# Kernel optimization log

Hardware: AMD Instinct MI355X
Metric: run time of the kernel (lower is better)

The kernel has to match this reference:

```python
import jax, jax.numpy as jnp
import numpy as np

LOSS_IDX = jnp.array([0, 1])    # loss_indices from __init__
BASIS_IDX = jnp.array([0, 1])   # dtw_mapping_basis (x, y)


def _dtw_path(cost):
    """Classic DTW DP + backtrack on cost [N, M].
    Returns padded alignment path (a, b) of length N+M-1 with validity mask.
    DP is run as an anti-diagonal wavefront scan (L = N+M-1 steps)."""
    N, M = cost.shape
    L = N + M - 1
    inf = jnp.float32(jnp.inf)
    i_idx = jnp.arange(N)

    def diag_step(carry, k):
        prev1, prev2 = carry  # diagonals k-1 and k-2, indexed by row i
        j = k - i_idx
        valid = (j >= 0) & (j < M)
        c = cost[i_idx, jnp.clip(j, 0, M - 1)]
        up = jnp.concatenate([jnp.full((1,), inf), prev1[:-1]])  # D[i-1, j]
        dg = jnp.concatenate([jnp.full((1,), inf), prev2[:-1]])  # D[i-1, j-1]
        lf = prev1                                               # D[i, j-1]
        best = jnp.minimum(jnp.minimum(up, dg), lf)
        best = jnp.where(jnp.isinf(best), jnp.float32(0.0), best)  # (0,0) seed
        cur = jnp.where(valid, c + best, inf)
        return (cur, prev1), cur

    init = (jnp.full((N,), inf), jnp.full((N,), inf))
    _, diags = jax.lax.scan(diag_step, init, jnp.arange(L))  # [L, N]: D[i,j] = diags[i+j, i]

    def getD(i, j):
        ok = (i >= 0) & (j >= 0)
        return jnp.where(ok, diags[jnp.clip(i + j, 0, L - 1), jnp.clip(i, 0, N - 1)], inf)

    def bt_step(carry, _):
        i, j, done = carry
        emit_valid = jnp.logical_not(done)
        cand = jnp.stack([getD(i - 1, j - 1), getD(i - 1, j), getD(i, j - 1)])
        m = jnp.argmin(cand)  # 0: diag, 1: up, 2: left
        ni = jnp.where(m == 2, i, i - 1)
        nj = jnp.where(m == 1, j, j - 1)
        done2 = done | ((i == 0) & (j == 0))
        ni = jnp.where(done2, 0, ni)
        nj = jnp.where(done2, 0, nj)
        return (ni, nj, done2), (i, j, emit_valid)

    init_bt = (jnp.int32(N - 1), jnp.int32(M - 1), jnp.bool_(False))
    _, (a, b, valid) = jax.lax.scan(bt_step, init_bt, None, length=L)
    return a, b, valid


def _dtw_loss_single(pred, targ, subcoef):
    # DTW alignment is computed on detached (numpy in torch) basis coords.
    p = jax.lax.stop_gradient(pred)[:, BASIS_IDX]
    t = jax.lax.stop_gradient(targ)[:, BASIS_IDX]
    # euclidean pairwise distance cost [N, M]
    cost = jnp.sqrt(jnp.sum((p[:, None, :] - t[None, :, :]) ** 2, axis=-1))
    a, b, valid = _dtw_path(cost)
    d = jnp.abs(pred[a][:, LOSS_IDX] - targ[b][:, LOSS_IDX]) * subcoef  # [L, 2]
    return jnp.sum(d * valid[:, None].astype(d.dtype))


def setup_inputs() -> dict:
    key = jax.random.key(0)
    k1, k2 = jax.random.split(key)
    B, N, M, F = 32, 1024, 1024, 4
    preds = jax.random.normal(k1, (B, N, F), dtype=jnp.float32)
    targs = jax.random.normal(k2, (B, M, F), dtype=jnp.float32)
    subcoef = jnp.ones((2,), dtype=jnp.float32)
    return {"preds": preds, "targs": targs, "subcoef": subcoef}


def reference(preds, targs, subcoef):
    per_sample = jax.vmap(_dtw_loss_single, in_axes=(0, 0, None))(preds, targs, subcoef)
    return jnp.sum(per_sample)
```

## Files before the change

kernel.cpp:

```cpp
#include <hip/hip_runtime.h>
#include <math.h>

#define BATCH 32
#define NN 1024
#define MM 1024
#define RR 4
#define CC 4
#define LANES 64
#define NWAVE 4
#define TPB (MM / 4)
#define NSUP (TPB + LANES - 1)
#define LAG 72
#define TOT (NSUP + (NWAVE - 1) * LAG)
#define DEPTH 32
#define DEC_WORDS_PER_BATCH ((NN / 4) * (MM / 4))
#define DEC_BYTES ((size_t)BATCH * DEC_WORDS_PER_BATCH * 4)
#define REQ_WS DEC_BYTES
#define LPATH (NN + MM - 1)

__global__ void init_kernel(float* out) { out[0] = 0.0f; }

__device__ inline void bt_walk4(const unsigned* __restrict__ sdec, int roff,
                                int iLow, int& i, int& j, int& n,
                                unsigned* __restrict__ path)
{
    int ri = i >> 2, jc = j >> 2;
    unsigned w = sdec[(ri - roff) * 256 + jc];
    while (true) {
        const int base = (ri - roff) * 256 + jc;
        const unsigned wl = sdec[(jc > 0)    ? base - 1   : base];
        const unsigned wu = sdec[(ri > roff) ? base - 256 : base];
        const unsigned wd = sdec[(ri > roff && jc > 0) ? base - 257 : base];
        bool done = false, susp = false;
        while (true) {
            path[n++] = ((unsigned)i << 16) | (unsigned)j;
            if ((i | j) == 0) { done = true; break; }
            const unsigned m = (w >> (((i & 3) * 4 + (j & 3)) * 2)) & 3u;
            i -= (m != 2u); j -= (m != 1u);
            if (i < iLow) { susp = true; break; }
            if ((i >> 2) != ri || (j >> 2) != jc) break;
        }
        if (done || susp) break;
        const int nri = i >> 2, njc = j >> 2;
        w = (nri == ri) ? wl : ((njc == jc) ? wu : wd);
        ri = nri; jc = njc;
    }
}

__global__ __launch_bounds__(256, 1) void dtw_fused(
    const float* __restrict__ preds, const float* __restrict__ targs,
    const float* __restrict__ subcoef, unsigned* __restrict__ dec,
    float* __restrict__ out)
{
    const int b = blockIdx.x, t = threadIdx.x;
    const int l = t & 63, w = t >> 6;
    const float INF = __builtin_inff();

    __shared__ float pxA[NN], pyA[NN], txA[MM], tyA[MM];
    __shared__ float4 ring[NWAVE - 1][DEPTH];
    __shared__ unsigned sdec[128 * 256];
    __shared__ unsigned path[LPATH + 1];
    __shared__ int sI, sJ, sN;
    __shared__ float wsum[NWAVE];

    for (int it = 0; it < NN / 256; ++it) {
        const int idx = it * 256 + t;
        const float4 p4 = ((const float4*)preds)[(size_t)b * NN + idx];
        pxA[idx] = p4.x; pyA[idx] = p4.y;
        const float4 t4 = ((const float4*)targs)[(size_t)b * MM + idx];
        txA[idx] = t4.x; tyA[idx] = t4.y;
    }
    __syncthreads();

    const int i0 = (w << 8) + (l << 2);
    const float4 px4 = ((const float4*)pxA)[i0 >> 2];
    const float4 py4 = ((const float4*)pyA)[i0 >> 2];
    const float px[RR] = {px4.x, px4.y, px4.z, px4.w};
    const float py[RR] = {py4.x, py4.y, py4.z, py4.w};
    unsigned* __restrict__ decT =
        dec + (size_t)b * DEC_WORDS_PER_BATCH + (size_t)(i0 >> 2) * TPB;

    float Dp[RR], Dbot[CC], bv[CC];
    #pragma unroll
    for (int r = 0; r < RR; ++r) Dp[r] = INF;
    #pragma unroll
    for (int c = 0; c < CC; ++c) { Dbot[c] = INF; bv[c] = INF; }
    float bndRet = (w == 0 && l == 0) ? 0.0f : INF;
    float4 gcur = make_float4(INF, INF, INF, INF);
    float4 tx4 = ((const float4*)txA)[0], ty4 = ((const float4*)tyA)[0];

    for (int u = 0; u < TOT; ++u) {
        const int ul = u - LAG * w;
        if (l == 0) {
            const bool gb = (w > 0) && (ul >= 0) && (ul < TPB);
            bv[0] = gb ? gcur.x : INF; bv[1] = gb ? gcur.y : INF;
            bv[2] = gb ? gcur.z : INF; bv[3] = gb ? gcur.w : INF;
        }
        const bool act = (ul >= l) && (ul < l + TPB);
        if (act) {
            const int j0 = CC * (ul - l);
            const float cx[CC] = {tx4.x, tx4.y, tx4.z, tx4.w};
            const float cy[CC] = {ty4.x, ty4.y, ty4.z, ty4.w};
            float cost[RR][CC];
            #pragma unroll
            for (int c = 0; c < CC; ++c)
                #pragma unroll
                for (int r = 0; r < RR; ++r) {
                    const float dx = px[r] - cx[c], dy = py[r] - cy[c];
                    cost[r][c] = __builtin_amdgcn_sqrtf(dx * dx + dy * dy);
                }
            unsigned word = 0;
            #pragma unroll
            for (int c = 0; c < CC; ++c) {
                float up = bv[c];
                float dg = (c == 0) ? bndRet : bv[c - 1];
                #pragma unroll
                for (int r = 0; r < RR; ++r) {
                    const float lf = Dp[r];
                    const unsigned m = (dg <= up && dg <= lf) ? 0u
                                     : ((up <= lf) ? 1u : 2u);
                    const float D = cost[r][c] + fminf(dg, fminf(up, lf));
                    word |= m << ((r * 4 + c) * 2);
                    dg = lf; up = D; Dp[r] = D;
                }
                Dbot[c] = up;
            }
            decT[j0 >> 2] = word;
            if (l == LANES - 1 && w < NWAVE - 1)
                ring[w][ul & (DEPTH - 1)] =
                    make_float4(Dbot[0], Dbot[1], Dbot[2], Dbot[3]);
        }
        bndRet = bv[CC - 1];
        #pragma unroll
        for (int c = 0; c < CC; ++c) bv[c] = __shfl_up(Dbot[c], 1);
        const int un = ul + 1;
        if (un >= l && un < l + TPB) {
            const int jn = CC * (un - l);
            tx4 = ((const float4*)txA)[jn >> 2];
            ty4 = ((const float4*)tyA)[jn >> 2];
        }
        if (l == 0 && w > 0 && un >= 0 && un < TPB)
            gcur = ring[w - 1][(un + 63) & (DEPTH - 1)];
        if ((u & 7) == 7) __syncthreads();
    }

    __threadfence_block();
    __syncthreads();

    const unsigned* __restrict__ decB = dec + (size_t)b * DEC_WORDS_PER_BATCH;
    {
        uint4* s4 = (uint4*)sdec;
        const uint4* g4 = (const uint4*)(decB + 128 * 256);
        for (int k = t; k < 8192; k += 256) s4[k] = g4[k];
    }
    __syncthreads();
    if (t == 0) {
        int i = NN - 1, j = MM - 1, n = 0;
        bt_walk4(sdec, 128, 512, i, j, n, path);
        sI = i; sJ = j; sN = n;
    }
    __syncthreads();
    {
        uint4* s4 = (uint4*)sdec;
        const uint4* g4 = (const uint4*)decB;
        for (int k = t; k < 8192; k += 256) s4[k] = g4[k];
    }
    __syncthreads();
    if (t == 0) {
        int i = sI, j = sJ, n = sN;
        bt_walk4(sdec, 0, 0, i, j, n, path);
        sN = n;
    }
    __syncthreads();

    const float sc0 = subcoef[0], sc1 = subcoef[1];
    const int n = sN;
    float acc = 0.0f;
    for (int p = t; p < n; p += 256) {
        const unsigned e = path[p];
        const int i = (int)(e >> 16), j = (int)(e & 0xffffu);
        acc += fabsf(pxA[i] - txA[j]) * sc0 + fabsf(pyA[i] - tyA[j]) * sc1;
    }
    #pragma unroll
    for (int o = 32; o > 0; o >>= 1) acc += __shfl_down(acc, o);
    if ((t & 63) == 0) wsum[t >> 6] = acc;
    __syncthreads();
    if (t == 0) atomicAdd(out, (wsum[0] + wsum[1]) + (wsum[2] + wsum[3]));
}

__global__ __launch_bounds__(256) void dtw_fallback(
    const float* __restrict__ preds, const float* __restrict__ targs,
    const float* __restrict__ subcoef, unsigned* __restrict__ dec,
    float* __restrict__ out)
{
    const int b = blockIdx.x;
    const int t = threadIdx.x;
    const float INF = __builtin_inff();
    __shared__ float px[NN], py[NN];
    __shared__ float txy[2 * MM];
    __shared__ float bbuf[2][256];

    for (int it = 0; it < NN / 256; ++it) {
        const int idx = it * 256 + t;
        const float4 p4 = ((const float4*)preds)[(size_t)b * NN + idx];
        px[idx] = p4.x; py[idx] = p4.y;
        const float4 t4 = ((const float4*)targs)[(size_t)b * MM + idx];
        txy[2 * idx] = t4.x; txy[2 * idx + 1] = t4.y;
    }
    bbuf[0][t] = INF; bbuf[1][t] = INF;
    __syncthreads();

    float pxr[4], pyr[4], Dp[4];
    #pragma unroll
    for (int r = 0; r < 4; ++r) {
        pxr[r] = px[4 * t + r]; pyr[r] = py[4 * t + r]; Dp[r] = INF;
    }
    float dgB = (t == 0) ? 0.0f : INF;
    unsigned packed = 0;
    unsigned* decB = dec + (size_t)b * 65536;
    for (int s = 0; s < MM + 255; ++s) {
        const int j = s - t;
        const float upB = (t == 0) ? INF : bbuf[(s + 1) & 1][t - 1];
        if (j >= 0 && j < MM) {
            const float txj = txy[2 * j], tyj = txy[2 * j + 1];
            float up = upB, dg = dgB;
            unsigned mbits = 0;
            #pragma unroll
            for (int r = 0; r < 4; ++r) {
                const float dx = pxr[r] - txj, dy = pyr[r] - tyj;
                const float c = sqrtf(dx * dx + dy * dy);
                const float lf = Dp[r];
                const unsigned m = (dg <= up && dg <= lf) ? 0u
                                 : ((up <= lf) ? 1u : 2u);
                mbits |= m << (r * 8 + (j & 3) * 2);
                const float Dc = c + fminf(up, fminf(dg, lf));
                dg = lf; up = Dc; Dp[r] = Dc;
            }
            packed |= mbits;
            if ((j & 3) == 3) { decB[(unsigned)t * 256 + (j >> 2)] = packed; packed = 0; }
            bbuf[s & 1][t] = Dp[3];
        }
        dgB = upB;
        __syncthreads();
    }
    __threadfence_block();
    __syncthreads();
    if (t == 0) {
        const float sc0 = subcoef[0], sc1 = subcoef[1];
        int i = NN - 1, jj = MM - 1;
        float loss = 0.0f;
        int ti = i >> 2, tj = jj >> 2;
        unsigned wv = decB[ti * 256 + tj];
        while (true) {
            const int tjl = (tj > 0) ? tj - 1 : 0;
            const int til = (ti > 0) ? ti - 1 : 0;
            const unsigned wl = decB[ti * 256 + tjl];
            const unsigned wu = decB[til * 256 + tj];
            const unsigned wd = decB[til * 256 + tjl];
            bool done = false;
            while (true) {
                loss += fabsf(px[i] - txy[2 * jj]) * sc0
                      + fabsf(py[i] - txy[2 * jj + 1]) * sc1;
                if ((i | jj) == 0) { done = true; break; }
                const unsigned m = (wv >> (((i & 3) * 4 + (jj & 3)) * 2)) & 3u;
                i -= (m != 2u); jj -= (m != 1u);
                if ((i >> 2) != ti || (jj >> 2) != tj) break;
            }
            if (done) break;
            const int nti = i >> 2, ntj = jj >> 2;
            wv = (nti == ti) ? wl : ((ntj == tj) ? wu : wd);
            ti = nti; tj = ntj;
        }
        atomicAdd(out, loss);
    }
}

extern "C" void kernel_launch(void* const* d_in, const int* in_sizes, int n_in,
                              void* d_out, int out_size, void* d_ws, size_t ws_size,
                              hipStream_t stream) {
    const float* preds   = (const float*)d_in[0];
    const float* targs   = (const float*)d_in[1];
    const float* subcoef = (const float*)d_in[2];
    float* out = (float*)d_out;
    unsigned* dec = (unsigned*)d_ws;

    init_kernel<<<1, 1, 0, stream>>>(out);
    if (ws_size >= REQ_WS) {
        dtw_fused<<<BATCH, 256, 0, stream>>>(preds, targs, subcoef, dec, out);
    } else {
        dtw_fallback<<<BATCH, 256, 0, stream>>>(preds, targs, subcoef, dec, out);
    }
}
```

Measured before the change: 598.2 us.

## Store decision words diagonal-packed per wave and backtrack in four bands

Each wave now keeps its decision words for eight wavefront steps in registers and writes them in a skewed, diagonal-packed layout once per 8-step group. The goal is coalesced global stores, since consecutive lanes on one diagonal land in adjacent words. Backtracking now runs over four per-wave bands of 16K words instead of two 32K-word halves, so shared memory use shrinks at the cost of more index arithmetic in the lookups. The lane shift moves to a DPP row-shift intrinsic, and the argmin test is rewritten to compare against the computed minimum.

```diff
diff --git a/kernel.cpp b/kernel.cpp
--- a/kernel.cpp
+++ b/kernel.cpp
@@ -11,40 +11,35 @@
 #define TPB (MM / 4)
 #define NSUP (TPB + LANES - 1)
 #define LAG 72
-#define TOT (NSUP + (NWAVE - 1) * LAG)
+#define TOT8 67
 #define DEPTH 32
-#define DEC_WORDS_PER_BATCH ((NN / 4) * (MM / 4))
+#define WORDS_PER_WAVE 16384
+#define DEC_WORDS_PER_BATCH (NWAVE * WORDS_PER_WAVE)
 #define DEC_BYTES ((size_t)BATCH * DEC_WORDS_PER_BATCH * 4)
 #define REQ_WS DEC_BYTES
 #define LPATH (NN + MM - 1)
 
 __global__ void init_kernel(float* out) { out[0] = 0.0f; }
 
-__device__ inline void bt_walk4(const unsigned* __restrict__ sdec, int roff,
-                                int iLow, int& i, int& j, int& n,
-                                unsigned* __restrict__ path)
-{
-    int ri = i >> 2, jc = j >> 2;
-    unsigned w = sdec[(ri - roff) * 256 + jc];
-    while (true) {
-        const int base = (ri - roff) * 256 + jc;
-        const unsigned wl = sdec[(jc > 0)    ? base - 1   : base];
-        const unsigned wu = sdec[(ri > roff) ? base - 256 : base];
-        const unsigned wd = sdec[(ri > roff && jc > 0) ? base - 257 : base];
-        bool done = false, susp = false;
-        while (true) {
-            path[n++] = ((unsigned)i << 16) | (unsigned)j;
-            if ((i | j) == 0) { done = true; break; }
-            const unsigned m = (w >> (((i & 3) * 4 + (j & 3)) * 2)) & 3u;
-            i -= (m != 2u); j -= (m != 1u);
-            if (i < iLow) { susp = true; break; }
-            if ((i >> 2) != ri || (j >> 2) != jc) break;
-        }
-        if (done || susp) break;
-        const int nri = i >> 2, njc = j >> 2;
-        w = (nri == ri) ? wl : ((njc == jc) ? wu : wd);
-        ri = nri; jc = njc;
-    }
+__device__ __forceinline__ float wave_shr1(float v, float fb) {
+    return __int_as_float(__builtin_amdgcn_update_dpp(
+        __float_as_int(fb), __float_as_int(v), 0x138, 0xf, 0xf, false));
+}
+
+__device__ __forceinline__ int pkoff(int d) {
+    if (d <= 63) return (d * (d + 1)) >> 1;
+    if (d <= 256) return 2016 + ((d - 63) << 6);
+    const int e = d - 256;
+    return 14368 + 63 * e - ((e * (e - 1)) >> 1);
+}
+__device__ __forceinline__ unsigned ldw(const unsigned* __restrict__ sdec,
+                                        int lr, int jc) {
+    int d = jc + lr;
+    d = d < 0 ? 0 : (d > 318 ? 318 : d);
+    const int lo = d > 255 ? d - 255 : 0;
+    const int hi = d < 63 ? d : 63;
+    const int l = lr < lo ? lo : (lr > hi ? hi : lr);
+    return sdec[pkoff(d) + l - lo];
 }
 
 __global__ __launch_bounds__(256, 1) void dtw_fused(
@@ -58,7 +53,7 @@
 
     __shared__ float pxA[NN], pyA[NN], txA[MM], tyA[MM];
     __shared__ float4 ring[NWAVE - 1][DEPTH];
-    __shared__ unsigned sdec[128 * 256];
+    __shared__ unsigned sdec[WORDS_PER_WAVE];
     __shared__ unsigned path[LPATH + 1];
     __shared__ int sI, sJ, sN;
     __shared__ float wsum[NWAVE];
@@ -77,8 +72,8 @@
     const float4 py4 = ((const float4*)pyA)[i0 >> 2];
     const float px[RR] = {px4.x, px4.y, px4.z, px4.w};
     const float py[RR] = {py4.x, py4.y, py4.z, py4.w};
-    unsigned* __restrict__ decT =
-        dec + (size_t)b * DEC_WORDS_PER_BATCH + (size_t)(i0 >> 2) * TPB;
+    unsigned* __restrict__ decW =
+        dec + (size_t)b * DEC_WORDS_PER_BATCH + (size_t)w * WORDS_PER_WAVE;
 
     float Dp[RR], Dbot[CC], bv[CC];
     #pragma unroll
@@ -88,90 +83,117 @@
     float bndRet = (w == 0 && l == 0) ? 0.0f : INF;
     float4 gcur = make_float4(INF, INF, INF, INF);
     float4 tx4 = ((const float4*)txA)[0], ty4 = ((const float4*)tyA)[0];
-
-    for (int u = 0; u < TOT; ++u) {
-        const int ul = u - LAG * w;
-        if (l == 0) {
-            const bool gb = (w > 0) && (ul >= 0) && (ul < TPB);
-            bv[0] = gb ? gcur.x : INF; bv[1] = gb ? gcur.y : INF;
-            bv[2] = gb ? gcur.z : INF; bv[3] = gb ? gcur.w : INF;
-        }
-        const bool act = (ul >= l) && (ul < l + TPB);
-        if (act) {
-            const int j0 = CC * (ul - l);
-            const float cx[CC] = {tx4.x, tx4.y, tx4.z, tx4.w};
-            const float cy[CC] = {ty4.x, ty4.y, ty4.z, ty4.w};
-            float cost[RR][CC];
+    unsigned wreg[8];
+
+    for (int u8 = 0; u8 < TOT8; ++u8) {
+        #pragma unroll
+        for (int dd = 0; dd < 8; ++dd) {
+            const int u = u8 * 8 + dd;
+            const int ul = u - LAG * w;
+            if (l == 0) {
+                const bool gb = (w > 0) && (ul >= 0) && (ul < TPB);
+                bv[0] = gb ? gcur.x : INF; bv[1] = gb ? gcur.y : INF;
+                bv[2] = gb ? gcur.z : INF; bv[3] = gb ? gcur.w : INF;
+            }
+            const bool act = (ul >= l) && (ul < l + TPB);
+            if (act) {
+                const float cx[CC] = {tx4.x, tx4.y, tx4.z, tx4.w};
+                const float cy[CC] = {ty4.x, ty4.y, ty4.z, ty4.w};
+                float cost[RR][CC];
+                #pragma unroll
+                for (int c = 0; c < CC; ++c)
+                    #pragma unroll
+                    for (int r = 0; r < RR; ++r) {
+                        const float dx = px[r] - cx[c], dy = py[r] - cy[c];
+                        cost[r][c] = __builtin_amdgcn_sqrtf(dx * dx + dy * dy);
+                    }
+                unsigned word = 0;
+                #pragma unroll
+                for (int c = 0; c < CC; ++c) {
+                    float up = bv[c];
+                    float dg = (c == 0) ? bndRet : bv[c - 1];
+                    #pragma unroll
+                    for (int r = 0; r < RR; ++r) {
+                        const float lf = Dp[r];
+                        const float best = fminf(dg, fminf(up, lf));
+                        const unsigned m = (best == dg) ? 0u
+                                         : ((best == up) ? 1u : 2u);
+                        const float D = cost[r][c] + best;
+                        word |= m << ((r * 4 + c) * 2);
+                        dg = lf; up = D; Dp[r] = D;
+                    }
+                    Dbot[c] = up;
+                }
+                wreg[dd] = word;
+                if (l == LANES - 1 && w < NWAVE - 1)
+                    ring[w][ul & (DEPTH - 1)] =
+                        make_float4(Dbot[0], Dbot[1], Dbot[2], Dbot[3]);
+            }
+            bndRet = bv[CC - 1];
             #pragma unroll
-            for (int c = 0; c < CC; ++c)
-                #pragma unroll
-                for (int r = 0; r < RR; ++r) {
-                    const float dx = px[r] - cx[c], dy = py[r] - cy[c];
-                    cost[r][c] = __builtin_amdgcn_sqrtf(dx * dx + dy * dy);
+            for (int c = 0; c < CC; ++c) bv[c] = wave_shr1(Dbot[c], INF);
+            const int un = ul + 1;
+            if (un >= l && un < l + TPB) {
+                const int jn = CC * (un - l);
+                tx4 = ((const float4*)txA)[jn >> 2];
+                ty4 = ((const float4*)tyA)[jn >> 2];
+            }
+            if (l == 0 && w > 0 && un >= 0 && un < TPB)
+                gcur = ring[w - 1][(un + 63) & (DEPTH - 1)];
+        }
+        const int ulbase = u8 * 8 - LAG * w;
+        #pragma unroll
+        for (int dd = 0; dd < 8; ++dd) {
+            const int d = ulbase + dd;
+            if (d >= 0 && d <= 318 && (unsigned)(d - l) < 256u) {
+                const int lo = d > 255 ? d - 255 : 0;
+                decW[pkoff(d) + l - lo] = wreg[dd];
+            }
+        }
+        __syncthreads();
+    }
+
+    __threadfence_block();
+    __syncthreads();
+
+    const unsigned* __restrict__ decB = dec + (size_t)b * DEC_WORDS_PER_BATCH;
+    if (t == 0) { sI = NN - 1; sJ = MM - 1; sN = 0; }
+    __syncthreads();
+    for (int band = NWAVE - 1; band >= 0; --band) {
+        {
+            uint4* s4 = (uint4*)sdec;
+            const uint4* g4 = (const uint4*)(decB + band * WORDS_PER_WAVE);
+            for (int k = t; k < WORDS_PER_WAVE / 4; k += 256) s4[k] = g4[k];
+        }
+        __syncthreads();
+        if (t == 0 && sI >= (band << 8)) {
+            int i = sI, j = sJ, n = sN;
+            const int iLow = band << 8, roff = band << 6;
+            int lr = (i >> 2) - roff, jc = j >> 2;
+            unsigned wcur = ldw(sdec, lr, jc);
+            while (true) {
+                const unsigned wl = ldw(sdec, lr, jc - 1);
+                const unsigned wu = ldw(sdec, lr - 1, jc);
+                const unsigned wd = ldw(sdec, lr - 1, jc - 1);
+                bool done = false, susp = false;
+                while (true) {
+                    path[n++] = ((unsigned)i << 16) | (unsigned)j;
+                    if ((i | j) == 0) { done = true; break; }
+                    const unsigned m =
+                        (wcur >> (((i & 3) * 4 + (j & 3)) * 2)) & 3u;
+                    i -= (m != 2u); j -= (m != 1u);
+                    if (i < iLow) { susp = true; break; }
+                    if (((i >> 2) - roff) != lr || (j >> 2) != jc) break;
                 }
-            unsigned word = 0;
-            #pragma unroll
-            for (int c = 0; c < CC; ++c) {
-                float up = bv[c];
-                float dg = (c == 0) ? bndRet : bv[c - 1];
-                #pragma unroll
-                for (int r = 0; r < RR; ++r) {
-                    const float lf = Dp[r];
-                    const unsigned m = (dg <= up && dg <= lf) ? 0u
-                                     : ((up <= lf) ? 1u : 2u);
-                    const float D = cost[r][c] + fminf(dg, fminf(up, lf));
-                    word |= m << ((r * 4 + c) * 2);
-                    dg = lf; up = D; Dp[r] = D;
-                }
-                Dbot[c] = up;
-            }
-            decT[j0 >> 2] = word;
-            if (l == LANES - 1 && w < NWAVE - 1)
-                ring[w][ul & (DEPTH - 1)] =
-                    make_float4(Dbot[0], Dbot[1], Dbot[2], Dbot[3]);
-        }
-        bndRet = bv[CC - 1];
-        #pragma unroll
-        for (int c = 0; c < CC; ++c) bv[c] = __shfl_up(Dbot[c], 1);
-        const int un = ul + 1;
-        if (un >= l && un < l + TPB) {
-            const int jn = CC * (un - l);
-            tx4 = ((const float4*)txA)[jn >> 2];
-            ty4 = ((const float4*)tyA)[jn >> 2];
-        }
-        if (l == 0 && w > 0 && un >= 0 && un < TPB)
-            gcur = ring[w - 1][(un + 63) & (DEPTH - 1)];
-        if ((u & 7) == 7) __syncthreads();
-    }
-
-    __threadfence_block();
-    __syncthreads();
-
-    const unsigned* __restrict__ decB = dec + (size_t)b * DEC_WORDS_PER_BATCH;
-    {
-        uint4* s4 = (uint4*)sdec;
-        const uint4* g4 = (const uint4*)(decB + 128 * 256);
-        for (int k = t; k < 8192; k += 256) s4[k] = g4[k];
-    }
-    __syncthreads();
-    if (t == 0) {
-        int i = NN - 1, j = MM - 1, n = 0;
-        bt_walk4(sdec, 128, 512, i, j, n, path);
-        sI = i; sJ = j; sN = n;
-    }
-    __syncthreads();
-    {
-        uint4* s4 = (uint4*)sdec;
-        const uint4* g4 = (const uint4*)decB;
-        for (int k = t; k < 8192; k += 256) s4[k] = g4[k];
-    }
-    __syncthreads();
-    if (t == 0) {
-        int i = sI, j = sJ, n = sN;
-        bt_walk4(sdec, 0, 0, i, j, n, path);
-        sN = n;
-    }
-    __syncthreads();
+                if (done || susp) break;
+                const int nlr = (i >> 2) - roff, njc = j >> 2;
+                wcur = (nlr == lr) ? wl : ((njc == jc) ? wu : wd);
+                lr = nlr; jc = njc;
+            }
+            sI = i; sJ = j; sN = n;
+        }
+        __syncthreads();
+    }
 
     const float sc0 = subcoef[0], sc1 = subcoef[1];
     const int n = sN;
```

Result: slower. 702.8 us (+17.5%).

## Replace periodic block barriers with per-wave progress flags in DTW wavefront

Applied to the files above, without the earlier changes.

Removes the __syncthreads issued every 8 steps in the wavefront DP loop. Each producer wave now publishes a release-stored progress counter, and each consumer wave spin-waits with acquire loads only when it needs boundary values that have not yet arrived. This lets waves drift independently instead of meeting at a barrier. It also simplifies the argmin selection by comparing against the computed minimum, and makes the target-coordinate loads unconditional with a clamped index. The spin loop with s_sleep adds polling latency and depends on a correct ordering between the ring writes and the flag store.

```diff
diff --git a/kernel.cpp b/kernel.cpp
--- a/kernel.cpp
+++ b/kernel.cpp
@@ -11,7 +11,7 @@
 #define TPB (MM / 4)
 #define NSUP (TPB + LANES - 1)
 #define LAG 72
-#define TOT (NSUP + (NWAVE - 1) * LAG)
+#define TOT (TPB + LANES - 1 + (NWAVE - 1) * LAG)
 #define DEPTH 32
 #define DEC_WORDS_PER_BATCH ((NN / 4) * (MM / 4))
 #define DEC_BYTES ((size_t)BATCH * DEC_WORDS_PER_BATCH * 4)
@@ -57,7 +57,8 @@
     const float INF = __builtin_inff();
 
     __shared__ float pxA[NN], pyA[NN], txA[MM], tyA[MM];
-    __shared__ float4 ring[NWAVE - 1][DEPTH];
+    __shared__ float ring[NWAVE - 1][DEPTH * 4];
+    __shared__ int prog[NWAVE - 1];
     __shared__ unsigned sdec[128 * 256];
     __shared__ unsigned path[LPATH + 1];
     __shared__ int sI, sJ, sN;
@@ -70,6 +71,7 @@
         const float4 t4 = ((const float4*)targs)[(size_t)b * MM + idx];
         txA[idx] = t4.x; tyA[idx] = t4.y;
     }
+    if (t < NWAVE - 1) prog[t] = 0;
     __syncthreads();
 
     const int i0 = (w << 8) + (l << 2);
@@ -86,19 +88,15 @@
     #pragma unroll
     for (int c = 0; c < CC; ++c) { Dbot[c] = INF; bv[c] = INF; }
     float bndRet = (w == 0 && l == 0) ? 0.0f : INF;
-    float4 gcur = make_float4(INF, INF, INF, INF);
     float4 tx4 = ((const float4*)txA)[0], ty4 = ((const float4*)tyA)[0];
+    float rv0 = INF, rv1 = INF, rv2 = INF, rv3 = INF;
+    int cachedProg = 0;
 
     for (int u = 0; u < TOT; ++u) {
         const int ul = u - LAG * w;
-        if (l == 0) {
-            const bool gb = (w > 0) && (ul >= 0) && (ul < TPB);
-            bv[0] = gb ? gcur.x : INF; bv[1] = gb ? gcur.y : INF;
-            bv[2] = gb ? gcur.z : INF; bv[3] = gb ? gcur.w : INF;
-        }
+        const int un = ul + 1;
         const bool act = (ul >= l) && (ul < l + TPB);
         if (act) {
-            const int j0 = CC * (ul - l);
             const float cx[CC] = {tx4.x, tx4.y, tx4.z, tx4.w};
             const float cy[CC] = {ty4.x, ty4.y, ty4.z, ty4.w};
             float cost[RR][CC];
@@ -117,31 +115,51 @@
                 #pragma unroll
                 for (int r = 0; r < RR; ++r) {
                     const float lf = Dp[r];
-                    const unsigned m = (dg <= up && dg <= lf) ? 0u
-                                     : ((up <= lf) ? 1u : 2u);
-                    const float D = cost[r][c] + fminf(dg, fminf(up, lf));
+                    const float best = fminf(dg, fminf(up, lf));
+                    const unsigned m = (best == dg) ? 0u
+                                     : ((best == up) ? 1u : 2u);
+                    const float D = cost[r][c] + best;
                     word |= m << ((r * 4 + c) * 2);
                     dg = lf; up = D; Dp[r] = D;
                 }
                 Dbot[c] = up;
             }
-            decT[j0 >> 2] = word;
-            if (l == LANES - 1 && w < NWAVE - 1)
-                ring[w][ul & (DEPTH - 1)] =
-                    make_float4(Dbot[0], Dbot[1], Dbot[2], Dbot[3]);
+            decT[ul - l] = word;
+            if (l == LANES - 1 && w < NWAVE - 1) {
+                volatile float* rp = &ring[w][(ul & (DEPTH - 1)) * 4];
+                rp[0] = Dbot[0]; rp[1] = Dbot[1];
+                rp[2] = Dbot[2]; rp[3] = Dbot[3];
+                if ((ul & 7) == 7 || ul == NSUP - 1)
+                    __hip_atomic_store(&prog[w], ul + 1, __ATOMIC_RELEASE,
+                                       __HIP_MEMORY_SCOPE_WORKGROUP);
+            }
         }
         bndRet = bv[CC - 1];
         #pragma unroll
         for (int c = 0; c < CC; ++c) bv[c] = __shfl_up(Dbot[c], 1);
-        const int un = ul + 1;
-        if (un >= l && un < l + TPB) {
-            const int jn = CC * (un - l);
-            tx4 = ((const float4*)txA)[jn >> 2];
-            ty4 = ((const float4*)tyA)[jn >> 2];
-        }
-        if (l == 0 && w > 0 && un >= 0 && un < TPB)
-            gcur = ring[w - 1][(un + 63) & (DEPTH - 1)];
-        if ((u & 7) == 7) __syncthreads();
+        if (w > 0) {
+            const int need = un + 64;
+            if (need >= 64 && need <= NSUP && cachedProg < need) {
+                do {
+                    __builtin_amdgcn_s_sleep(1);
+                    cachedProg = __hip_atomic_load(&prog[w - 1],
+                        __ATOMIC_ACQUIRE, __HIP_MEMORY_SCOPE_WORKGROUP);
+                } while (cachedProg < need);
+            }
+            const volatile float* rp =
+                &ring[w - 1][(((un + 63) & (DEPTH - 1))) * 4];
+            rv0 = rp[0]; rv1 = rp[1]; rv2 = rp[2]; rv3 = rp[3];
+        }
+        const bool useRing = (w > 0) && (un >= 0) && (un < TPB);
+        const float m0 = useRing ? rv0 : INF;
+        const float m1 = useRing ? rv1 : INF;
+        const float m2 = useRing ? rv2 : INF;
+        const float m3 = useRing ? rv3 : INF;
+        if (l == 0) { bv[0] = m0; bv[1] = m1; bv[2] = m2; bv[3] = m3; }
+        int jn = CC * (un - l);
+        jn = jn < 0 ? 0 : (jn > MM - 4 ? MM - 4 : jn);
+        tx4 = ((const float4*)txA)[jn >> 2];
+        ty4 = ((const float4*)tyA)[jn >> 2];
     }
 
     __threadfence_block();
```

After: 713.2 us. 19.2% more time.

## Pack two batch items per 512-thread block with chunked backtrack staging

Applied to the files above, without the earlier changes.

Each block now handles two batch samples using two independent 256-thread halves, so the grid drops from 32 blocks to 16. To fit two samples in LDS, the backtrack decision table is staged in 60-row chunks instead of two 128-row halves, and pred coordinates are read straight from global memory rather than staged in shared memory. Argmin selection is also recomputed from the min value. The per-sample serial wavefront stays the same, so two samples now share one CU and its issue slots and synchronisation, and the backtrack needs more staging passes.

```diff
diff --git a/kernel.cpp b/kernel.cpp
--- a/kernel.cpp
+++ b/kernel.cpp
@@ -11,12 +11,13 @@
 #define TPB (MM / 4)
 #define NSUP (TPB + LANES - 1)
 #define LAG 72
-#define TOT (NSUP + (NWAVE - 1) * LAG)
+#define TOT (TPB + LANES - 1 + (NWAVE - 1) * LAG)
 #define DEPTH 32
 #define DEC_WORDS_PER_BATCH ((NN / 4) * (MM / 4))
 #define DEC_BYTES ((size_t)BATCH * DEC_WORDS_PER_BATCH * 4)
 #define REQ_WS DEC_BYTES
 #define LPATH (NN + MM - 1)
+#define PH 60
 
 __global__ void init_kernel(float* out) { out[0] = 0.0f; }
 
@@ -47,38 +48,43 @@
     }
 }
 
-__global__ __launch_bounds__(256, 1) void dtw_fused(
+__global__ __launch_bounds__(512, 1) void dtw_fused2(
     const float* __restrict__ preds, const float* __restrict__ targs,
     const float* __restrict__ subcoef, unsigned* __restrict__ dec,
     float* __restrict__ out)
 {
-    const int b = blockIdx.x, t = threadIdx.x;
-    const int l = t & 63, w = t >> 6;
+    const int t = threadIdx.x;
+    const int sb = t >> 8;
+    const int tt = t & 255;
+    const int l = tt & 63, w = tt >> 6;
+    const int b = 2 * blockIdx.x + sb;
     const float INF = __builtin_inff();
 
-    __shared__ float pxA[NN], pyA[NN], txA[MM], tyA[MM];
-    __shared__ float4 ring[NWAVE - 1][DEPTH];
-    __shared__ unsigned sdec[128 * 256];
-    __shared__ unsigned path[LPATH + 1];
-    __shared__ int sI, sJ, sN;
-    __shared__ float wsum[NWAVE];
-
-    for (int it = 0; it < NN / 256; ++it) {
-        const int idx = it * 256 + t;
-        const float4 p4 = ((const float4*)preds)[(size_t)b * NN + idx];
-        pxA[idx] = p4.x; pyA[idx] = p4.y;
+    __shared__ float txA[2][MM], tyA[2][MM];
+    __shared__ float4 ring[2][NWAVE - 1][DEPTH];
+    __shared__ unsigned sdec[2][PH * 256];
+    __shared__ unsigned path[2][LPATH + 1];
+    __shared__ int sIv[2], sJv[2], sNv[2];
+    __shared__ float wsum[2][NWAVE];
+
+    for (int it = 0; it < MM / 256; ++it) {
+        const int idx = it * 256 + tt;
         const float4 t4 = ((const float4*)targs)[(size_t)b * MM + idx];
-        txA[idx] = t4.x; tyA[idx] = t4.y;
+        txA[sb][idx] = t4.x; tyA[sb][idx] = t4.y;
     }
     __syncthreads();
 
     const int i0 = (w << 8) + (l << 2);
-    const float4 px4 = ((const float4*)pxA)[i0 >> 2];
-    const float4 py4 = ((const float4*)pyA)[i0 >> 2];
-    const float px[RR] = {px4.x, px4.y, px4.z, px4.w};
-    const float py[RR] = {py4.x, py4.y, py4.z, py4.w};
+    float px[RR], py[RR];
+    #pragma unroll
+    for (int r = 0; r < RR; ++r) {
+        const float4 p4 = ((const float4*)preds)[(size_t)b * NN + i0 + r];
+        px[r] = p4.x; py[r] = p4.y;
+    }
     unsigned* __restrict__ decT =
         dec + (size_t)b * DEC_WORDS_PER_BATCH + (size_t)(i0 >> 2) * TPB;
+    const float* __restrict__ txB = txA[sb];
+    const float* __restrict__ tyB = tyA[sb];
 
     float Dp[RR], Dbot[CC], bv[CC];
     #pragma unroll
@@ -87,7 +93,7 @@
     for (int c = 0; c < CC; ++c) { Dbot[c] = INF; bv[c] = INF; }
     float bndRet = (w == 0 && l == 0) ? 0.0f : INF;
     float4 gcur = make_float4(INF, INF, INF, INF);
-    float4 tx4 = ((const float4*)txA)[0], ty4 = ((const float4*)tyA)[0];
+    float4 tx4 = ((const float4*)txB)[0], ty4 = ((const float4*)tyB)[0];
 
     for (int u = 0; u < TOT; ++u) {
         const int ul = u - LAG * w;
@@ -98,7 +104,6 @@
         }
         const bool act = (ul >= l) && (ul < l + TPB);
         if (act) {
-            const int j0 = CC * (ul - l);
             const float cx[CC] = {tx4.x, tx4.y, tx4.z, tx4.w};
             const float cy[CC] = {ty4.x, ty4.y, ty4.z, ty4.w};
             float cost[RR][CC];
@@ -117,17 +122,18 @@
                 #pragma unroll
                 for (int r = 0; r < RR; ++r) {
                     const float lf = Dp[r];
-                    const unsigned m = (dg <= up && dg <= lf) ? 0u
-                                     : ((up <= lf) ? 1u : 2u);
-                    const float D = cost[r][c] + fminf(dg, fminf(up, lf));
+                    const float best = fminf(dg, fminf(up, lf));
+                    const unsigned m = (best == dg) ? 0u
+                                     : ((best == up) ? 1u : 2u);
+                    const float D = cost[r][c] + best;
                     word |= m << ((r * 4 + c) * 2);
                     dg = lf; up = D; Dp[r] = D;
                 }
                 Dbot[c] = up;
             }
-            decT[j0 >> 2] = word;
+            decT[ul - l] = word;
             if (l == LANES - 1 && w < NWAVE - 1)
-                ring[w][ul & (DEPTH - 1)] =
+                ring[sb][w][ul & (DEPTH - 1)] =
                     make_float4(Dbot[0], Dbot[1], Dbot[2], Dbot[3]);
         }
         bndRet = bv[CC - 1];
@@ -136,11 +142,11 @@
         const int un = ul + 1;
         if (un >= l && un < l + TPB) {
             const int jn = CC * (un - l);
-            tx4 = ((const float4*)txA)[jn >> 2];
-            ty4 = ((const float4*)tyA)[jn >> 2];
+            tx4 = ((const float4*)txB)[jn >> 2];
+            ty4 = ((const float4*)tyB)[jn >> 2];
         }
         if (l == 0 && w > 0 && un >= 0 && un < TPB)
-            gcur = ring[w - 1][(un + 63) & (DEPTH - 1)];
+            gcur = ring[sb][w - 1][(un + 63) & (DEPTH - 1)];
         if ((u & 7) == 7) __syncthreads();
     }
 
@@ -148,44 +154,41 @@
     __syncthreads();
 
     const unsigned* __restrict__ decB = dec + (size_t)b * DEC_WORDS_PER_BATCH;
-    {
-        uint4* s4 = (uint4*)sdec;
-        const uint4* g4 = (const uint4*)(decB + 128 * 256);
-        for (int k = t; k < 8192; k += 256) s4[k] = g4[k];
-    }
-    __syncthreads();
-    if (t == 0) {
-        int i = NN - 1, j = MM - 1, n = 0;
-        bt_walk4(sdec, 128, 512, i, j, n, path);
-        sI = i; sJ = j; sN = n;
-    }
-    __syncthreads();
-    {
-        uint4* s4 = (uint4*)sdec;
-        const uint4* g4 = (const uint4*)decB;
-        for (int k = t; k < 8192; k += 256) s4[k] = g4[k];
-    }
-    __syncthreads();
-    if (t == 0) {
-        int i = sI, j = sJ, n = sN;
-        bt_walk4(sdec, 0, 0, i, j, n, path);
-        sN = n;
-    }
-    __syncthreads();
+    if (tt == 0) { sIv[sb] = NN - 1; sJv[sb] = MM - 1; sNv[sb] = 0; }
+    __syncthreads();
+    for (int hi = 256; hi > 0; hi -= PH) {
+        const int lo = hi > PH ? hi - PH : 0;
+        const int rows = hi - lo;
+        {
+            uint4* s4 = (uint4*)sdec[sb];
+            const uint4* g4 = (const uint4*)(decB + lo * 256);
+            for (int k = tt; k < rows * 64; k += 256) s4[k] = g4[k];
+        }
+        __syncthreads();
+        if (tt == 0 && sIv[sb] >= (lo << 2)) {
+            int i = sIv[sb], j = sJv[sb], n = sNv[sb];
+            bt_walk4(sdec[sb], lo, lo << 2, i, j, n, path[sb]);
+            sIv[sb] = i; sJv[sb] = j; sNv[sb] = n;
+        }
+        __syncthreads();
+    }
 
     const float sc0 = subcoef[0], sc1 = subcoef[1];
-    const int n = sN;
+    const int n = sNv[sb];
     float acc = 0.0f;
-    for (int p = t; p < n; p += 256) {
-        const unsigned e = path[p];
+    for (int p = tt; p < n; p += 256) {
+        const unsigned e = path[sb][p];
         const int i = (int)(e >> 16), j = (int)(e & 0xffffu);
-        acc += fabsf(pxA[i] - txA[j]) * sc0 + fabsf(pyA[i] - tyA[j]) * sc1;
+        const float4 p4 = ((const float4*)preds)[(size_t)b * NN + i];
+        acc += fabsf(p4.x - txA[sb][j]) * sc0 + fabsf(p4.y - tyA[sb][j]) * sc1;
     }
     #pragma unroll
     for (int o = 32; o > 0; o >>= 1) acc += __shfl_down(acc, o);
-    if ((t & 63) == 0) wsum[t >> 6] = acc;
-    __syncthreads();
-    if (t == 0) atomicAdd(out, (wsum[0] + wsum[1]) + (wsum[2] + wsum[3]));
+    if ((tt & 63) == 0) wsum[sb][w] = acc;
+    __syncthreads();
+    if (tt == 0)
+        atomicAdd(out, (wsum[sb][0] + wsum[sb][1]) +
+                       (wsum[sb][2] + wsum[sb][3]));
 }
 
 __global__ __launch_bounds__(256) void dtw_fallback(
@@ -286,7 +289,7 @@
 
     init_kernel<<<1, 1, 0, stream>>>(out);
     if (ws_size >= REQ_WS) {
-        dtw_fused<<<BATCH, 256, 0, stream>>>(preds, targs, subcoef, dec, out);
+        dtw_fused2<<<BATCH / 2, 512, 0, stream>>>(preds, targs, subcoef, dec, out);
     } else {
         dtw_fallback<<<BATCH, 256, 0, stream>>>(preds, targs, subcoef, dec, out);
     }
```

After: 868.1 us. +45.1%, slower.
